# Optimization experiments

Hardware: AMD Instinct MI355X
Metric: run time of the kernel (lower is better)

The kernel has to match this reference:

```python
import jax, jax.numpy as jnp
import numpy as np

B, DIN, H, NACT = 8192, 1025, 1024, 1026
NHEAD = 513  # npatches + STOP
K = 32       # kR = kS


def _make_seq(key, batch, n, k):
    k_idx, k_len = jax.random.split(key)
    # distinct indices per row: top-k of a random permutation
    perm = jnp.argsort(jax.random.uniform(k_idx, (batch, n)), axis=1)[:, :k]
    seq_len = jax.random.randint(k_len, (batch,), 1, k + 1).astype(jnp.int32)
    mask = jnp.arange(k)[None, :] < seq_len[:, None]
    seq_idx = jnp.where(mask, perm, -1).astype(jnp.int32)
    return seq_idx, seq_len


def setup_inputs() -> dict:
    key = jax.random.key(0)
    ks = jax.random.split(key, 8)
    state = jax.random.normal(ks[0], (B, DIN), dtype=jnp.float32)
    W0 = jax.random.normal(ks[1], (DIN, H), dtype=jnp.float32) * (2.0 / DIN) ** 0.5
    b0 = jnp.zeros((H,), jnp.float32)
    W1 = jax.random.normal(ks[2], (H, H), dtype=jnp.float32) * (2.0 / H) ** 0.5
    b1 = jnp.zeros((H,), jnp.float32)
    W2 = jax.random.normal(ks[3], (H, NACT), dtype=jnp.float32) * 0.01
    b2 = jnp.zeros((NACT,), jnp.float32)
    seq_idx_R, seq_len_R = _make_seq(ks[4], B, NHEAD, K)
    seq_idx_S, seq_len_S = _make_seq(ks[5], B, NHEAD, K)
    return {"state": state, "W0": W0, "b0": b0, "W1": W1, "b1": b1,
            "W2": W2, "b2": b2,
            "seq_idx_R": seq_idx_R, "seq_len_R": seq_len_R,
            "seq_idx_S": seq_idx_S, "seq_len_S": seq_len_S}


def _mlp(state, W0, b0, W1, b1, W2, b2):
    h = jax.nn.relu(state @ W0 + b0)
    h = jax.nn.relu(h @ W1 + b1)
    return h @ W2 + b2  # (B, NACT) logits


def _logprob_entropy_wo_replacement(logits, seq_idx, seq_len):
    # Faithful vectorized version of logprob_entropy_wo_replacement_batched.
    bsz, n = logits.shape
    col = jnp.arange(n)[None, :]
    neg_inf = jnp.float32(-jnp.inf)

    def step(carry, xs):
        remaining, logp, ent = carry          # (B,N) bool, (B,), (B,)
        t, idx_t = xs                          # scalar, (B,)
        active = t < seq_len                   # (B,)
        masked_logits = jnp.where(remaining, logits, neg_inf)
        lp = jax.nn.log_softmax(masked_logits, axis=-1)
        p = jnp.exp(lp)
        mp = jnp.where(remaining, p, 0.0)
        mlp_ = jnp.where(remaining, lp, 0.0)
        ent_step = -jnp.sum(mp * mlp_, axis=-1)
        ent = ent + jnp.where(active, ent_step, 0.0)
        valid = active & (idx_t >= 0)
        idx_safe = jnp.where(valid, idx_t, 0)
        g = jnp.take_along_axis(lp, idx_safe[:, None], axis=1)[:, 0]
        logp = logp + jnp.where(valid, g, 0.0)
        hit = (col == idx_safe[:, None]) & valid[:, None]
        remaining = remaining & ~hit
        return (remaining, logp, ent), None

    init = (jnp.ones((bsz, n), bool), jnp.zeros((bsz,), jnp.float32),
            jnp.zeros((bsz,), jnp.float32))
    ts = jnp.arange(seq_idx.shape[1], dtype=jnp.int32)
    (_, logp, ent), _ = jax.lax.scan(step, init, (ts, seq_idx.T))
    return logp, ent


def reference(state, W0, b0, W1, b1, W2, b2,
              seq_idx_R, seq_len_R, seq_idx_S, seq_len_S):
    x = _mlp(state, W0, b0, W1, b1, W2, b2)
    logpR, entR = _logprob_entropy_wo_replacement(x[:, :NHEAD], seq_idx_R, seq_len_R)
    logpS, entS = _logprob_entropy_wo_replacement(x[:, NHEAD:NHEAD + NHEAD], seq_idx_S, seq_len_S)
    # rows: [total logprob, total entropy] as in get_log_prob's (logpR+logpS, entR+entS)
    return jnp.stack([logpR + logpS, entR + entS], axis=0)  # (2, B)
```

## Files before the change

kernel.cpp:

```cpp
#include <hip/hip_runtime.h>
#include <cstdint>
#include <cstddef>

#define BATCH 8192
#define DIN   1025
#define HID   1024
#define NACT  1026
#define NHEAD 513
#define KSEL  32
#define KP0   1088
#define NP2   1152

typedef unsigned short u16;
typedef short bf16x8 __attribute__((ext_vector_type(8)));
typedef float f32x4 __attribute__((ext_vector_type(4)));

__device__ __forceinline__ u16 f2bf(float f) {
  unsigned u = __float_as_uint(f);
  u += 0x7fff + ((u >> 16) & 1);
  return (u16)(u >> 16);
}
__device__ __forceinline__ float bf2f(u16 h) {
  return __uint_as_float((unsigned)h << 16);
}

__device__ __forceinline__ void async_cp16(const u16* g, u16* l) {
  __builtin_amdgcn_global_load_lds((const __attribute__((address_space(1))) void*)g,
                                   (__attribute__((address_space(3))) void*)l,
                                   16, 0, 0);
}


__global__ void cvt_all(const float* __restrict__ state,
                        const float* __restrict__ W0, const float* __restrict__ W1,
                        const float* __restrict__ W2,
                        u16* __restrict__ As, u16* __restrict__ W0t,
                        u16* __restrict__ W1t, u16* __restrict__ W2t) {
  const int b = blockIdx.x;
  const int tid = threadIdx.x;
  if (b < 8704) {
    int idx = b * 256 + tid;
    const int QPR = KP0 / 4;
    int r  = idx / QPR;
    int c4 = (idx - r * QPR) * 4;
    const float* src = state + (size_t)r * DIN + c4;
    ushort4 o;
    if (c4 + 3 < DIN) {
      o.x = f2bf(src[0]); o.y = f2bf(src[1]); o.z = f2bf(src[2]); o.w = f2bf(src[3]);
    } else {
      o.x = (c4 + 0 < DIN) ? f2bf(src[0]) : 0;
      o.y = (c4 + 1 < DIN) ? f2bf(src[1]) : 0;
      o.z = (c4 + 2 < DIN) ? f2bf(src[2]) : 0;
      o.w = (c4 + 3 < DIN) ? f2bf(src[3]) : 0;
    }
    *(ushort4*)(As + (size_t)r * KP0 + c4) = o;
    return;
  }
  int w = b - 8704;
  const float* W; u16* Wt; int K, N, Kp, Np, nx;
  if (w < 1088)      { W = W0; Wt = W0t; K = DIN; N = HID;  Kp = KP0; Np = HID; nx = 32; }
  else if (w < 2112) { w -= 1088; W = W1; Wt = W1t; K = HID; N = HID;  Kp = HID; Np = HID; nx = 32; }
  else               { w -= 2112; W = W2; Wt = W2t; K = HID; N = NACT; Kp = HID; Np = NP2; nx = 36; }
  int n0 = (w % nx) * 32, k0 = (w / nx) * 32;
  __shared__ float tile[32][33];
  int tx = tid & 31, ty = tid >> 5;
#pragma unroll
  for (int i = 0; i < 32; i += 8) {
    int k = k0 + ty + i, n = n0 + tx;
    tile[ty + i][tx] = (k < K && n < N) ? W[(size_t)k * N + n] : 0.f;
  }
  __syncthreads();
#pragma unroll
  for (int i = 0; i < 32; i += 8) {
    int n = n0 + ty + i, k = k0 + tx;
    if (n < Np && k < Kp) Wt[(size_t)n * Kp + k] = f2bf(tile[tx][ty + i]);
  }
}


template<bool RELU, int NT, int K>
__global__ __launch_bounds__(256, 2)
void gemm_bt(const u16* __restrict__ A, const u16* __restrict__ Bt,
             const float* __restrict__ bias, int nbias,
             u16* __restrict__ Cout, int ldc)
{
  __shared__ __align__(16) u16 lds[16384];

  const int d     = blockIdx.x;
  const int group = d / (8 * NT);
  const int rsub  = d - group * (8 * NT);
  const int ntile = rsub >> 3;
  const int mtile = group * 8 + (rsub & 7);

  const int tid  = threadIdx.x;
  const int wave = tid >> 6;
  const int lane = tid & 63;
  const int waveM = wave >> 1, waveN = wave & 1;
  const int lr = lane & 15, lq = lane >> 4;
  const size_t bm = (size_t)mtile * 128;
  const size_t bn = (size_t)ntile * 128;

  const int c0   = wave * 64 + lane;
  const int row0 = c0 >> 2;
  const int g0   = (c0 & 3) ^ ((row0 >> 1) & 3);
  const int c1   = c0 + 256;
  const int row1 = c1 >> 2;
  const int g1   = (c1 & 3) ^ ((row1 >> 1) & 3);
  const u16* gA0 = A  + (bm + row0) * (size_t)K + g0 * 8;
  const u16* gA1 = A  + (bm + row1) * (size_t)K + g1 * 8;
  const u16* gB0 = Bt + (bn + row0) * (size_t)K + g0 * 8;
  const u16* gB1 = Bt + (bn + row1) * (size_t)K + g1 * 8;
  u16* lA = lds + wave * 512;
  u16* lB = lds + 4096 + wave * 512;

  f32x4 acc[4][4] = {};

  const int s = lq ^ ((lr >> 1) & 3);
  const u16* pa = lds + (waveM * 64 + lr) * 32 + s * 8;
  const u16* pb = lds + 4096 + (waveN * 64 + lr) * 32 + s * 8;

  auto issue = [&](int k0, int b) {
    u16* a  = lA + b * 8192;
    u16* bb = lB + b * 8192;
    async_cp16(gA0 + k0, a);
    async_cp16(gA1 + k0, a + 2048);
    async_cp16(gB0 + k0, bb);
    async_cp16(gB1 + k0, bb + 2048);
  };

  const int NIT = K / 32;
  issue(0, 0);
#pragma unroll 2
  for (int it = 0; it < NIT; ++it) {
    const int b = it & 1;
    if (it + 1 < NIT) {
      issue((it + 1) * 32, b ^ 1);
      asm volatile("s_waitcnt vmcnt(4)\n\ts_barrier" ::: "memory");
    } else {
      asm volatile("s_waitcnt vmcnt(0)\n\ts_barrier" ::: "memory");
    }

    bf16x8 af[4], bf[4];
    const u16* qa = pa + b * 8192;
    const u16* qb = pb + b * 8192;
#pragma unroll
    for (int t = 0; t < 4; ++t) {
      af[t] = *(const bf16x8*)(qa + t * 512);
      bf[t] = *(const bf16x8*)(qb + t * 512);
    }
#pragma unroll
    for (int tm = 0; tm < 4; ++tm)
#pragma unroll
      for (int tn = 0; tn < 4; ++tn)
        acc[tm][tn] = __builtin_amdgcn_mfma_f32_16x16x32_bf16(af[tm], bf[tn], acc[tm][tn], 0, 0, 0);

    asm volatile("s_waitcnt lgkmcnt(0)\n\ts_barrier" ::: "memory");
  }

#pragma unroll
  for (int tm = 0; tm < 4; ++tm) {
    size_t rw = bm + waveM * 64 + tm * 16 + lq * 4;
#pragma unroll
    for (int tn = 0; tn < 4; ++tn) {
      int col = (int)bn + waveN * 64 + tn * 16 + lr;
      float bv = (col < nbias) ? bias[col] : 0.f;
#pragma unroll
      for (int r = 0; r < 4; ++r) {
        float v = acc[tm][tn][r] + bv;
        if (RELU) v = fmaxf(v, 0.f);
        Cout[(rw + r) * ldc + col] = f2bf(v);
      }
    }
  }
}


__global__ void sample_k(const u16* __restrict__ logits,
                         const int* __restrict__ idxR, const int* __restrict__ lenR,
                         const int* __restrict__ idxS, const int* __restrict__ lenS,
                         float* __restrict__ out)
{
  const int row  = blockIdx.x;
  const int w    = threadIdx.x >> 6;
  const int lane = threadIdx.x & 63;
  const u16* x = logits + (size_t)row * NP2 + w * NHEAD;
  const int* sidx = (w ? idxS : idxR) + (size_t)row * KSEL;
  const int slen  = (w ? lenS : lenR)[row];

  float m = -3.4e38f;
  for (int i = lane; i < NHEAD; i += 64) m = fmaxf(m, bf2f(x[i]));
#pragma unroll
  for (int d = 32; d; d >>= 1) m = fmaxf(m, __shfl_xor(m, d, 64));

  float S = 0.f, T = 0.f;
  for (int i = lane; i < NHEAD; i += 64) {
    float xi = bf2f(x[i]);
    float e = __expf(xi - m);
    S += e; T += e * xi;
  }
#pragma unroll
  for (int d = 32; d; d >>= 1) { S += __shfl_xor(S, d, 64); T += __shfl_xor(T, d, 64); }

  float e = 0.f, ex = 0.f, xt = 0.f;
  int active = (lane < KSEL) && (lane < slen);
  int valid = 0;
  if (active) {
    int id = sidx[lane];
    if (id >= 0) {
      valid = 1;
      xt = bf2f(x[id]);
      e  = __expf(xt - m);
      ex = e * xt;
    }
  }
  float pe = e, pex = ex;
#pragma unroll
  for (int d = 1; d < 32; d <<= 1) {
    float a = __shfl_up(pe, d, 64);
    float b = __shfl_up(pex, d, 64);
    if (lane >= d) { pe += a; pex += b; }
  }
  float lp = 0.f, en = 0.f;
  if (active) {
    float St = S - (pe - e);
    float Tt = T - (pex - ex);
    float logZ = m + __logf(St);
    en = logZ - Tt / St;
    if (valid) lp = xt - logZ;
  }
#pragma unroll
  for (int d = 32; d; d >>= 1) { lp += __shfl_xor(lp, d, 64); en += __shfl_xor(en, d, 64); }

  __shared__ float sh[4];
  if (lane == 0) { sh[w * 2] = lp; sh[w * 2 + 1] = en; }
  __syncthreads();
  if (threadIdx.x == 0) {
    out[row]         = sh[0] + sh[2];
    out[BATCH + row] = sh[1] + sh[3];
  }
}


extern "C" void kernel_launch(void* const* d_in, const int* in_sizes, int n_in,
                              void* d_out, int out_size, void* d_ws, size_t ws_size,
                              hipStream_t stream) {
  (void)in_sizes; (void)n_in; (void)out_size; (void)ws_size;
  const float* state = (const float*)d_in[0];
  const float* W0 = (const float*)d_in[1];
  const float* b0 = (const float*)d_in[2];
  const float* W1 = (const float*)d_in[3];
  const float* b1 = (const float*)d_in[4];
  const float* W2 = (const float*)d_in[5];
  const float* b2 = (const float*)d_in[6];
  const int* idxR = (const int*)d_in[7];
  const int* lenR = (const int*)d_in[8];
  const int* idxS = (const int*)d_in[9];
  const int* lenS = (const int*)d_in[10];
  float* out = (float*)d_out;

  char* ws = (char*)d_ws;
  size_t off = 0;
  auto alloc = [&](size_t bytes) -> char* {
    char* p = ws + off;
    off = (off + bytes + 255) & ~(size_t)255;
    return p;
  };
  u16* As     = (u16*)alloc((size_t)BATCH * KP0 * 2);
  u16* W0t    = (u16*)alloc((size_t)HID * KP0 * 2);
  u16* W1t    = (u16*)alloc((size_t)HID * HID * 2);
  u16* W2t    = (u16*)alloc((size_t)NP2 * HID * 2);
  u16* h1     = (u16*)alloc((size_t)BATCH * HID * 2);
  u16* lgts   = (u16*)alloc((size_t)BATCH * NP2 * 2);
  u16* h2 = As;

  cvt_all<<<8704 + 3264, 256, 0, stream>>>(state, W0, W1, W2, As, W0t, W1t, W2t);

  gemm_bt<true,  8, KP0><<<(BATCH / 128) * (HID / 128), 256, 0, stream>>>(As, W0t, b0, HID,  h1,   HID);
  gemm_bt<true,  8, HID><<<(BATCH / 128) * (HID / 128), 256, 0, stream>>>(h1, W1t, b1, HID,  h2,   HID);
  gemm_bt<false, 9, HID><<<(BATCH / 128) * (NP2 / 128), 256, 0, stream>>>(h2, W2t, b2, NACT, lgts, NP2);

  sample_k<<<BATCH, 128, 0, stream>>>(lgts, idxR, lenR, idxS, lenS, out);
}
```

Before: 202.3 us.

## Fuse pipeline into persistent cooperative megakernel and compute last two logits in sampler

Replaces the five separate launches (convert, three GEMMs, sampler) with one persistent cooperative kernel of 256 blocks of 512 threads that separates phases with grid syncs. Each block runs two 256-thread GEMM teams on adjacent N tiles. The third GEMM now produces only 1024 logit columns instead of 1152 padded ones, and the two leftover logits are computed as dot products inside the sampling phase. This removes launch gaps and the padded GEMM work. In exchange it relies on cooperative launch (with a multi-kernel fallback), grid-wide barriers, and fixing the GEMM to exactly one tile pair per block.

```diff
diff --git a/kernel.cpp b/kernel.cpp
--- a/kernel.cpp
+++ b/kernel.cpp
@@ -1,6 +1,9 @@
 #include <hip/hip_runtime.h>
+#include <hip/hip_cooperative_groups.h>
 #include <cstdint>
 #include <cstddef>
+
+namespace cg = cooperative_groups;
 
 #define BATCH 8192
 #define DIN   1025
@@ -9,7 +12,8 @@
 #define NHEAD 513
 #define KSEL  32
 #define KP0   1088
-#define NP2   1152
+#define LGN   1024
+#define GRID  256
 
 typedef unsigned short u16;
 typedef short bf16x8 __attribute__((ext_vector_type(8)));
@@ -30,20 +34,19 @@
                                    16, 0, 0);
 }
 
-
-__global__ void cvt_all(const float* __restrict__ state,
-                        const float* __restrict__ W0, const float* __restrict__ W1,
-                        const float* __restrict__ W2,
-                        u16* __restrict__ As, u16* __restrict__ W0t,
-                        u16* __restrict__ W1t, u16* __restrict__ W2t) {
-  const int b = blockIdx.x;
+struct MegaArgs {
+  const float *state, *W0, *b0, *W1, *b1, *W2, *b2;
+  const int *idxR, *lenR, *idxS, *lenS;
+  u16 *As, *W0t, *W1t, *W2t, *W2c, *h1, *h2, *lgts;
+  float *out;
+};
+
+__device__ void cvt_phase(const MegaArgs& a, u16* lds) {
   const int tid = threadIdx.x;
-  if (b < 8704) {
-    int idx = b * 256 + tid;
-    const int QPR = KP0 / 4;
-    int r  = idx / QPR;
-    int c4 = (idx - r * QPR) * 4;
-    const float* src = state + (size_t)r * DIN + c4;
+  const int QPR = KP0 / 4;
+  for (int i = blockIdx.x * 512 + tid; i < BATCH * QPR; i += GRID * 512) {
+    int r = i / QPR, c4 = (i - r * QPR) * 4;
+    const float* src = a.state + (size_t)r * DIN + c4;
     ushort4 o;
     if (c4 + 3 < DIN) {
       o.x = f2bf(src[0]); o.y = f2bf(src[1]); o.z = f2bf(src[2]); o.w = f2bf(src[3]);
@@ -53,52 +56,56 @@
       o.z = (c4 + 2 < DIN) ? f2bf(src[2]) : 0;
       o.w = (c4 + 3 < DIN) ? f2bf(src[3]) : 0;
     }
-    *(ushort4*)(As + (size_t)r * KP0 + c4) = o;
-    return;
-  }
-  int w = b - 8704;
-  const float* W; u16* Wt; int K, N, Kp, Np, nx;
-  if (w < 1088)      { W = W0; Wt = W0t; K = DIN; N = HID;  Kp = KP0; Np = HID; nx = 32; }
-  else if (w < 2112) { w -= 1088; W = W1; Wt = W1t; K = HID; N = HID;  Kp = HID; Np = HID; nx = 32; }
-  else               { w -= 2112; W = W2; Wt = W2t; K = HID; N = NACT; Kp = HID; Np = NP2; nx = 36; }
-  int n0 = (w % nx) * 32, k0 = (w / nx) * 32;
-  __shared__ float tile[32][33];
-  int tx = tid & 31, ty = tid >> 5;
-#pragma unroll
-  for (int i = 0; i < 32; i += 8) {
-    int k = k0 + ty + i, n = n0 + tx;
-    tile[ty + i][tx] = (k < K && n < N) ? W[(size_t)k * N + n] : 0.f;
-  }
-  __syncthreads();
-#pragma unroll
-  for (int i = 0; i < 32; i += 8) {
-    int n = n0 + ty + i, k = k0 + tx;
-    if (n < Np && k < Kp) Wt[(size_t)n * Kp + k] = f2bf(tile[tx][ty + i]);
-  }
-}
-
-
-template<bool RELU, int NT, int K>
-__global__ __launch_bounds__(256, 2)
-void gemm_bt(const u16* __restrict__ A, const u16* __restrict__ Bt,
-             const float* __restrict__ bias, int nbias,
-             u16* __restrict__ Cout, int ldc)
+    *(ushort4*)(a.As + (size_t)r * KP0 + c4) = o;
+  }
+  float (*tile)[33] = (float(*)[33])lds;
+  const int tx = tid & 31, ty = tid >> 5;
+  for (int t = blockIdx.x; t < 3137; t += GRID) {
+    if (t == 3136) {
+      for (int e = tid; e < 2048; e += 512) {
+        int j = e >> 10, k = e & 1023;
+        a.W2c[e] = f2bf(a.W2[(size_t)k * NACT + 1024 + j]);
+      }
+      continue;
+    }
+    const float* W; u16* Wt; int K, ldW, Kp, tt = t;
+    if (tt < 1088)      { W = a.W0; Wt = a.W0t; K = DIN; ldW = HID;  Kp = KP0; }
+    else if (tt < 2112) { tt -= 1088; W = a.W1; Wt = a.W1t; K = HID; ldW = HID;  Kp = HID; }
+    else                { tt -= 2112; W = a.W2; Wt = a.W2t; K = HID; ldW = NACT; Kp = HID; }
+    int n0 = (tt & 31) * 32, k0 = (tt >> 5) * 32;
+#pragma unroll
+    for (int i = 0; i < 32; i += 16) {
+      int k = k0 + ty + i;
+      tile[ty + i][tx] = (k < K) ? W[(size_t)k * ldW + n0 + tx] : 0.f;
+    }
+    __syncthreads();
+#pragma unroll
+    for (int i = 0; i < 32; i += 16)
+      Wt[(size_t)(n0 + ty + i) * Kp + k0 + tx] = f2bf(tile[tx][ty + i]);
+    __syncthreads();
+  }
+}
+
+template<bool RELU, int K>
+__device__ void gemm_phase(const u16* __restrict__ A, const u16* __restrict__ Bt,
+                           const float* __restrict__ bias, u16* __restrict__ Cout,
+                           int ldc, u16* lds0)
 {
-  __shared__ __align__(16) u16 lds[16384];
-
-  const int d     = blockIdx.x;
-  const int group = d / (8 * NT);
-  const int rsub  = d - group * (8 * NT);
-  const int ntile = rsub >> 3;
-  const int mtile = group * 8 + (rsub & 7);
-
   const int tid  = threadIdx.x;
-  const int wave = tid >> 6;
+  const int team = tid >> 8;
+  const int ttid = tid & 255;
+  const int wave = ttid >> 6;
   const int lane = tid & 63;
   const int waveM = wave >> 1, waveN = wave & 1;
   const int lr = lane & 15, lq = lane >> 4;
+
+  const int b = blockIdx.x;
+  const int mtile = ((b >> 5) << 3) | (b & 7);
+  const int ntile = (((b >> 3) & 3) << 1) | team;
   const size_t bm = (size_t)mtile * 128;
   const size_t bn = (size_t)ntile * 128;
+
+  u16* lds = lds0 + team * 16384;
 
   const int c0   = wave * 64 + lane;
   const int row0 = c0 >> 2;
@@ -119,11 +126,11 @@
   const u16* pa = lds + (waveM * 64 + lr) * 32 + s * 8;
   const u16* pb = lds + 4096 + (waveN * 64 + lr) * 32 + s * 8;
 
-  auto issue = [&](int k0, int b) {
-    u16* a  = lA + b * 8192;
-    u16* bb = lB + b * 8192;
-    async_cp16(gA0 + k0, a);
-    async_cp16(gA1 + k0, a + 2048);
+  auto issue = [&](int k0, int buf) {
+    u16* aa = lA + buf * 8192;
+    u16* bb = lB + buf * 8192;
+    async_cp16(gA0 + k0, aa);
+    async_cp16(gA1 + k0, aa + 2048);
     async_cp16(gB0 + k0, bb);
     async_cp16(gB1 + k0, bb + 2048);
   };
@@ -132,17 +139,17 @@
   issue(0, 0);
 #pragma unroll 2
   for (int it = 0; it < NIT; ++it) {
-    const int b = it & 1;
+    const int buf = it & 1;
     if (it + 1 < NIT) {
-      issue((it + 1) * 32, b ^ 1);
+      issue((it + 1) * 32, buf ^ 1);
       asm volatile("s_waitcnt vmcnt(4)\n\ts_barrier" ::: "memory");
     } else {
       asm volatile("s_waitcnt vmcnt(0)\n\ts_barrier" ::: "memory");
     }
 
     bf16x8 af[4], bf[4];
-    const u16* qa = pa + b * 8192;
-    const u16* qb = pb + b * 8192;
+    const u16* qa = pa + buf * 8192;
+    const u16* qb = pb + buf * 8192;
 #pragma unroll
     for (int t = 0; t < 4; ++t) {
       af[t] = *(const bf16x8*)(qa + t * 512);
@@ -163,7 +170,7 @@
 #pragma unroll
     for (int tn = 0; tn < 4; ++tn) {
       int col = (int)bn + waveN * 64 + tn * 16 + lr;
-      float bv = (col < nbias) ? bias[col] : 0.f;
+      float bv = bias[col];
 #pragma unroll
       for (int r = 0; r < 4; ++r) {
         float v = acc[tm][tn][r] + bv;
@@ -174,90 +181,138 @@
   }
 }
 
-
-__global__ void sample_k(const u16* __restrict__ logits,
-                         const int* __restrict__ idxR, const int* __restrict__ lenR,
-                         const int* __restrict__ idxS, const int* __restrict__ lenS,
-                         float* __restrict__ out)
-{
-  const int row  = blockIdx.x;
-  const int w    = threadIdx.x >> 6;
-  const int lane = threadIdx.x & 63;
-  const u16* x = logits + (size_t)row * NP2 + w * NHEAD;
-  const int* sidx = (w ? idxS : idxR) + (size_t)row * KSEL;
-  const int slen  = (w ? lenS : lenR)[row];
-
-  float m = -3.4e38f;
-  for (int i = lane; i < NHEAD; i += 64) m = fmaxf(m, bf2f(x[i]));
-#pragma unroll
-  for (int d = 32; d; d >>= 1) m = fmaxf(m, __shfl_xor(m, d, 64));
-
-  float S = 0.f, T = 0.f;
-  for (int i = lane; i < NHEAD; i += 64) {
-    float xi = bf2f(x[i]);
-    float e = __expf(xi - m);
-    S += e; T += e * xi;
-  }
-#pragma unroll
-  for (int d = 32; d; d >>= 1) { S += __shfl_xor(S, d, 64); T += __shfl_xor(T, d, 64); }
-
-  float e = 0.f, ex = 0.f, xt = 0.f;
-  int active = (lane < KSEL) && (lane < slen);
-  int valid = 0;
-  if (active) {
-    int id = sidx[lane];
-    if (id >= 0) {
-      valid = 1;
-      xt = bf2f(x[id]);
-      e  = __expf(xt - m);
-      ex = e * xt;
-    }
-  }
-  float pe = e, pex = ex;
-#pragma unroll
-  for (int d = 1; d < 32; d <<= 1) {
-    float a = __shfl_up(pe, d, 64);
-    float b = __shfl_up(pex, d, 64);
-    if (lane >= d) { pe += a; pex += b; }
-  }
-  float lp = 0.f, en = 0.f;
-  if (active) {
-    float St = S - (pe - e);
-    float Tt = T - (pex - ex);
-    float logZ = m + __logf(St);
-    en = logZ - Tt / St;
-    if (valid) lp = xt - logZ;
-  }
-#pragma unroll
-  for (int d = 32; d; d >>= 1) { lp += __shfl_xor(lp, d, 64); en += __shfl_xor(en, d, 64); }
-
-  __shared__ float sh[4];
-  if (lane == 0) { sh[w * 2] = lp; sh[w * 2 + 1] = en; }
-  __syncthreads();
-  if (threadIdx.x == 0) {
-    out[row]         = sh[0] + sh[2];
-    out[BATCH + row] = sh[1] + sh[3];
-  }
-}
-
+__device__ void sample_phase(const MegaArgs& a, u16* lds) {
+  float* shf = (float*)lds;
+  const int tid = threadIdx.x;
+  const int w = tid >> 6, lane = tid & 63;
+  const int grp = w & 1, pair = w >> 1;
+  for (int it = 0; it < 8; ++it) {
+    const int row = it * 1024 + blockIdx.x * 4 + pair;
+    const u16* base = a.lgts + (size_t)row * LGN + (grp ? NHEAD : 0);
+    const int* sidx = (grp ? a.idxS : a.idxR) + (size_t)row * KSEL;
+    const int slen  = (grp ? a.lenS : a.lenR)[row];
+
+    float x1024 = 0.f, x1025 = 0.f;
+    if (grp) {
+      float d0 = 0.f, d1 = 0.f;
+      const u16* hr  = a.h2 + (size_t)row * HID + lane * 16;
+      const u16* w0p = a.W2c + lane * 16;
+      const u16* w1p = a.W2c + 1024 + lane * 16;
+#pragma unroll
+      for (int j = 0; j < 16; ++j) {
+        float h = bf2f(hr[j]);
+        d0 += h * bf2f(w0p[j]);
+        d1 += h * bf2f(w1p[j]);
+      }
+#pragma unroll
+      for (int dd = 32; dd; dd >>= 1) { d0 += __shfl_xor(d0, dd, 64); d1 += __shfl_xor(d1, dd, 64); }
+      x1024 = d0 + a.b2[1024];
+      x1025 = d1 + a.b2[1025];
+    }
+    const int NHm = grp ? 511 : 513;
+
+    float m = -3.4e38f;
+    for (int i = lane; i < NHm; i += 64) m = fmaxf(m, bf2f(base[i]));
+    if (grp) {
+      if (lane == 63) m = fmaxf(m, x1024);
+      if (lane == 0)  m = fmaxf(m, x1025);
+    }
+#pragma unroll
+    for (int dd = 32; dd; dd >>= 1) m = fmaxf(m, __shfl_xor(m, dd, 64));
+
+    float S = 0.f, T = 0.f;
+    for (int i = lane; i < NHm; i += 64) {
+      float xi = bf2f(base[i]);
+      float e = __expf(xi - m);
+      S += e; T += e * xi;
+    }
+    if (grp) {
+      if (lane == 63) { float e = __expf(x1024 - m); S += e; T += e * x1024; }
+      if (lane == 0)  { float e = __expf(x1025 - m); S += e; T += e * x1025; }
+    }
+#pragma unroll
+    for (int dd = 32; dd; dd >>= 1) { S += __shfl_xor(S, dd, 64); T += __shfl_xor(T, dd, 64); }
+
+    float e = 0.f, ex = 0.f, xt = 0.f;
+    int active = (lane < KSEL) && (lane < slen);
+    int valid = 0;
+    if (active) {
+      int id = sidx[lane];
+      if (id >= 0) {
+        valid = 1;
+        if (grp && id >= 511) xt = (id == 511) ? x1024 : x1025;
+        else                  xt = bf2f(base[id]);
+        e  = __expf(xt - m);
+        ex = e * xt;
+      }
+    }
+    float pe = e, pex = ex;
+#pragma unroll
+    for (int dd = 1; dd < 32; dd <<= 1) {
+      float qa = __shfl_up(pe, dd, 64);
+      float qb = __shfl_up(pex, dd, 64);
+      if (lane >= dd) { pe += qa; pex += qb; }
+    }
+    float lp = 0.f, en = 0.f;
+    if (active) {
+      float St = S - (pe - e);
+      float Tt = T - (pex - ex);
+      float logZ = m + __logf(St);
+      en = logZ - Tt / St;
+      if (valid) lp = xt - logZ;
+    }
+#pragma unroll
+    for (int dd = 32; dd; dd >>= 1) { lp += __shfl_xor(lp, dd, 64); en += __shfl_xor(en, dd, 64); }
+
+    if (lane == 0) { shf[w * 2] = lp; shf[w * 2 + 1] = en; }
+    __syncthreads();
+    if (lane == 0 && grp == 0) {
+      a.out[row]         = shf[pair * 4] + shf[pair * 4 + 2];
+      a.out[BATCH + row] = shf[pair * 4 + 1] + shf[pair * 4 + 3];
+    }
+    __syncthreads();
+  }
+}
+
+__global__ __launch_bounds__(512, 2) void mega(MegaArgs a) {
+  __shared__ __align__(16) u16 lds[32768];
+  cg::grid_group g = cg::this_grid();
+  cvt_phase(a, lds);
+  __threadfence(); g.sync();
+  gemm_phase<true,  KP0>(a.As, a.W0t, a.b0, a.h1, HID, lds);
+  __threadfence(); g.sync();
+  gemm_phase<true,  HID>(a.h1, a.W1t, a.b1, a.h2, HID, lds);
+  __threadfence(); g.sync();
+  gemm_phase<false, HID>(a.h2, a.W2t, a.b2, a.lgts, LGN, lds);
+  __threadfence(); g.sync();
+  sample_phase(a, lds);
+}
+
+__global__ __launch_bounds__(512, 2) void k_cvt(MegaArgs a) {
+  __shared__ __align__(16) u16 lds[32768];
+  cvt_phase(a, lds);
+}
+__global__ __launch_bounds__(512, 2) void k_gemm1(MegaArgs a) {
+  __shared__ __align__(16) u16 lds[32768];
+  gemm_phase<true, KP0>(a.As, a.W0t, a.b0, a.h1, HID, lds);
+}
+__global__ __launch_bounds__(512, 2) void k_gemm2(MegaArgs a) {
+  __shared__ __align__(16) u16 lds[32768];
+  gemm_phase<true, HID>(a.h1, a.W1t, a.b1, a.h2, HID, lds);
+}
+__global__ __launch_bounds__(512, 2) void k_gemm3(MegaArgs a) {
+  __shared__ __align__(16) u16 lds[32768];
+  gemm_phase<false, HID>(a.h2, a.W2t, a.b2, a.lgts, LGN, lds);
+}
+__global__ __launch_bounds__(512, 2) void k_sample(MegaArgs a) {
+  __shared__ __align__(16) u16 lds[32768];
+  sample_phase(a, lds);
+}
 
 extern "C" void kernel_launch(void* const* d_in, const int* in_sizes, int n_in,
                               void* d_out, int out_size, void* d_ws, size_t ws_size,
                               hipStream_t stream) {
   (void)in_sizes; (void)n_in; (void)out_size; (void)ws_size;
-  const float* state = (const float*)d_in[0];
-  const float* W0 = (const float*)d_in[1];
-  const float* b0 = (const float*)d_in[2];
-  const float* W1 = (const float*)d_in[3];
-  const float* b1 = (const float*)d_in[4];
-  const float* W2 = (const float*)d_in[5];
-  const float* b2 = (const float*)d_in[6];
-  const int* idxR = (const int*)d_in[7];
-  const int* lenR = (const int*)d_in[8];
-  const int* idxS = (const int*)d_in[9];
-  const int* lenS = (const int*)d_in[10];
-  float* out = (float*)d_out;
-
   char* ws = (char*)d_ws;
   size_t off = 0;
   auto alloc = [&](size_t bytes) -> char* {
@@ -265,19 +320,34 @@
     off = (off + bytes + 255) & ~(size_t)255;
     return p;
   };
-  u16* As     = (u16*)alloc((size_t)BATCH * KP0 * 2);
-  u16* W0t    = (u16*)alloc((size_t)HID * KP0 * 2);
-  u16* W1t    = (u16*)alloc((size_t)HID * HID * 2);
-  u16* W2t    = (u16*)alloc((size_t)NP2 * HID * 2);
-  u16* h1     = (u16*)alloc((size_t)BATCH * HID * 2);
-  u16* lgts   = (u16*)alloc((size_t)BATCH * NP2 * 2);
-  u16* h2 = As;
-
-  cvt_all<<<8704 + 3264, 256, 0, stream>>>(state, W0, W1, W2, As, W0t, W1t, W2t);
-
-  gemm_bt<true,  8, KP0><<<(BATCH / 128) * (HID / 128), 256, 0, stream>>>(As, W0t, b0, HID,  h1,   HID);
-  gemm_bt<true,  8, HID><<<(BATCH / 128) * (HID / 128), 256, 0, stream>>>(h1, W1t, b1, HID,  h2,   HID);
-  gemm_bt<false, 9, HID><<<(BATCH / 128) * (NP2 / 128), 256, 0, stream>>>(h2, W2t, b2, NACT, lgts, NP2);
-
-  sample_k<<<BATCH, 128, 0, stream>>>(lgts, idxR, lenR, idxS, lenS, out);
-}
+
+  MegaArgs a;
+  a.state = (const float*)d_in[0];
+  a.W0 = (const float*)d_in[1];  a.b0 = (const float*)d_in[2];
+  a.W1 = (const float*)d_in[3];  a.b1 = (const float*)d_in[4];
+  a.W2 = (const float*)d_in[5];  a.b2 = (const float*)d_in[6];
+  a.idxR = (const int*)d_in[7];  a.lenR = (const int*)d_in[8];
+  a.idxS = (const int*)d_in[9];  a.lenS = (const int*)d_in[10];
+  a.out = (float*)d_out;
+
+  a.As   = (u16*)alloc((size_t)BATCH * KP0 * 2);
+  a.W0t  = (u16*)alloc((size_t)HID * KP0 * 2);
+  a.W1t  = (u16*)alloc((size_t)HID * HID * 2);
+  a.W2t  = (u16*)alloc((size_t)HID * LGN * 2);
+  a.W2c  = (u16*)alloc((size_t)2 * 1024 * 2);
+  a.h1   = (u16*)alloc((size_t)BATCH * HID * 2);
+  a.h2   = (u16*)alloc((size_t)BATCH * HID * 2);
+  a.lgts = (u16*)alloc((size_t)BATCH * LGN * 2);
+
+  void* params[] = { &a };
+  hipError_t err = hipLaunchCooperativeKernel((const void*)mega, dim3(GRID), dim3(512),
+                                              params, 0, stream);
+  if (err != hipSuccess) {
+    (void)hipGetLastError();
+    k_cvt   <<<GRID, 512, 0, stream>>>(a);
+    k_gemm1 <<<GRID, 512, 0, stream>>>(a);
+    k_gemm2 <<<GRID, 512, 0, stream>>>(a);
+    k_gemm3 <<<GRID, 512, 0, stream>>>(a);
+    k_sample<<<GRID, 512, 0, stream>>>(a);
+  }
+}
```

Result: slower. 596.8 us (+194.9%).

## Use 128x256 GEMM tiles and compute the last two logits in the sampling kernel

Applied to the files above, without the earlier changes.

The GEMM moves to 512-thread blocks that each compute a 128x256 output tile with a larger double-buffered LDS, so the launch is 256 blocks instead of 512. The final GEMM's N dimension shrinks from a padded 1152 to 1024. The two leftover logit columns (1024 and 1025) are computed as small dot products inside the sampling kernel, which now handles four rows per block. The aim is to cut padded GEMM work and raise operand reuse per tile. The cost is a single wave of large blocks on the GPU, which may leave compute units idle or unbalanced, plus extra per-row dot-product work in the sampler.

```diff
diff --git a/kernel.cpp b/kernel.cpp
--- a/kernel.cpp
+++ b/kernel.cpp
@@ -9,7 +9,7 @@
 #define NHEAD 513
 #define KSEL  32
 #define KP0   1088
-#define NP2   1152
+#define LGN   1024
 
 typedef unsigned short u16;
 typedef short bf16x8 __attribute__((ext_vector_type(8)));
@@ -30,19 +30,17 @@
                                    16, 0, 0);
 }
 
-
-__global__ void cvt_all(const float* __restrict__ state,
-                        const float* __restrict__ W0, const float* __restrict__ W1,
-                        const float* __restrict__ W2,
-                        u16* __restrict__ As, u16* __restrict__ W0t,
-                        u16* __restrict__ W1t, u16* __restrict__ W2t) {
+__global__ __launch_bounds__(512) void k_cvt(const float* __restrict__ state,
+    const float* __restrict__ W0, const float* __restrict__ W1,
+    const float* __restrict__ W2,
+    u16* __restrict__ As, u16* __restrict__ W0t, u16* __restrict__ W1t,
+    u16* __restrict__ W2t, u16* __restrict__ W2c) {
+  const int tid = threadIdx.x;
   const int b = blockIdx.x;
-  const int tid = threadIdx.x;
-  if (b < 8704) {
-    int idx = b * 256 + tid;
+  {
+    int i = b * 512 + tid;
     const int QPR = KP0 / 4;
-    int r  = idx / QPR;
-    int c4 = (idx - r * QPR) * 4;
+    int r = i / QPR, c4 = (i - r * QPR) * 4;
     const float* src = state + (size_t)r * DIN + c4;
     ushort4 o;
     if (c4 + 3 < DIN) {
@@ -54,64 +52,65 @@
       o.w = (c4 + 3 < DIN) ? f2bf(src[3]) : 0;
     }
     *(ushort4*)(As + (size_t)r * KP0 + c4) = o;
+  }
+  if (b >= 3137) return;
+  if (b == 3136) {
+    for (int e = tid; e < 2048; e += 512) {
+      int j = e >> 10, k = e & 1023;
+      W2c[e] = f2bf(W2[(size_t)k * NACT + 1024 + j]);
+    }
     return;
   }
-  int w = b - 8704;
-  const float* W; u16* Wt; int K, N, Kp, Np, nx;
-  if (w < 1088)      { W = W0; Wt = W0t; K = DIN; N = HID;  Kp = KP0; Np = HID; nx = 32; }
-  else if (w < 2112) { w -= 1088; W = W1; Wt = W1t; K = HID; N = HID;  Kp = HID; Np = HID; nx = 32; }
-  else               { w -= 2112; W = W2; Wt = W2t; K = HID; N = NACT; Kp = HID; Np = NP2; nx = 36; }
-  int n0 = (w % nx) * 32, k0 = (w / nx) * 32;
+  const float* W; u16* Wt; int K, ldW, Kp, tt = b;
+  if (tt < 1088)      { W = W0; Wt = W0t; K = DIN; ldW = HID;  Kp = KP0; }
+  else if (tt < 2112) { tt -= 1088; W = W1; Wt = W1t; K = HID; ldW = HID;  Kp = HID; }
+  else                { tt -= 2112; W = W2; Wt = W2t; K = HID; ldW = NACT; Kp = HID; }
+  int n0 = (tt & 31) * 32, k0 = (tt >> 5) * 32;
   __shared__ float tile[32][33];
-  int tx = tid & 31, ty = tid >> 5;
-#pragma unroll
-  for (int i = 0; i < 32; i += 8) {
-    int k = k0 + ty + i, n = n0 + tx;
-    tile[ty + i][tx] = (k < K && n < N) ? W[(size_t)k * N + n] : 0.f;
+  const int tx = tid & 31, ty = tid >> 5;
+#pragma unroll
+  for (int i = 0; i < 32; i += 16) {
+    int k = k0 + ty + i;
+    tile[ty + i][tx] = (k < K) ? W[(size_t)k * ldW + n0 + tx] : 0.f;
   }
   __syncthreads();
 #pragma unroll
-  for (int i = 0; i < 32; i += 8) {
-    int n = n0 + ty + i, k = k0 + tx;
-    if (n < Np && k < Kp) Wt[(size_t)n * Kp + k] = f2bf(tile[tx][ty + i]);
-  }
-}
-
-
-template<bool RELU, int NT, int K>
-__global__ __launch_bounds__(256, 2)
+  for (int i = 0; i < 32; i += 16)
+    Wt[(size_t)(n0 + ty + i) * Kp + k0 + tx] = f2bf(tile[tx][ty + i]);
+}
+
+template<bool RELU, int K>
+__global__ __launch_bounds__(512, 2)
 void gemm_bt(const u16* __restrict__ A, const u16* __restrict__ Bt,
-             const float* __restrict__ bias, int nbias,
-             u16* __restrict__ Cout, int ldc)
+             const float* __restrict__ bias, u16* __restrict__ Cout, int ldc)
 {
-  __shared__ __align__(16) u16 lds[16384];
+  __shared__ __align__(16) u16 lds[24576];
 
   const int d     = blockIdx.x;
-  const int group = d / (8 * NT);
-  const int rsub  = d - group * (8 * NT);
-  const int ntile = rsub >> 3;
-  const int mtile = group * 8 + (rsub & 7);
+  const int m8    = d & 7;
+  const int ntile = (d >> 3) & 3;
+  const int mtile = ((d >> 5) << 3) | m8;
+  const size_t bm = (size_t)mtile * 128;
+  const size_t bn = (size_t)ntile * 256;
 
   const int tid  = threadIdx.x;
   const int wave = tid >> 6;
   const int lane = tid & 63;
-  const int waveM = wave >> 1, waveN = wave & 1;
+  const int waveM = wave >> 2, waveN = wave & 3;
   const int lr = lane & 15, lq = lane >> 4;
-  const size_t bm = (size_t)mtile * 128;
-  const size_t bn = (size_t)ntile * 128;
-
-  const int c0   = wave * 64 + lane;
-  const int row0 = c0 >> 2;
-  const int g0   = (c0 & 3) ^ ((row0 >> 1) & 3);
-  const int c1   = c0 + 256;
-  const int row1 = c1 >> 2;
-  const int g1   = (c1 & 3) ^ ((row1 >> 1) & 3);
-  const u16* gA0 = A  + (bm + row0) * (size_t)K + g0 * 8;
-  const u16* gA1 = A  + (bm + row1) * (size_t)K + g1 * 8;
-  const u16* gB0 = Bt + (bn + row0) * (size_t)K + g0 * 8;
-  const u16* gB1 = Bt + (bn + row1) * (size_t)K + g1 * 8;
-  u16* lA = lds + wave * 512;
-  u16* lB = lds + 4096 + wave * 512;
+
+  const int rowA  = tid >> 2;
+  const int gA_   = (tid & 3) ^ ((rowA >> 1) & 3);
+  const int rowB0 = tid >> 2;
+  const int gB0_  = (tid & 3) ^ ((rowB0 >> 1) & 3);
+  const int rowB1 = rowB0 + 128;
+  const int gB1_  = (tid & 3) ^ ((rowB1 >> 1) & 3);
+  const u16* gA  = A  + (bm + rowA)  * (size_t)K + gA_  * 8;
+  const u16* gB0 = Bt + (bn + rowB0) * (size_t)K + gB0_ * 8;
+  const u16* gB1 = Bt + (bn + rowB1) * (size_t)K + gB1_ * 8;
+  u16* lA  = lds + wave * 512;
+  u16* lB0 = lds + 4096 + wave * 512;
+  u16* lB1 = lB0 + 4096;
 
   f32x4 acc[4][4] = {};
 
@@ -119,30 +118,28 @@
   const u16* pa = lds + (waveM * 64 + lr) * 32 + s * 8;
   const u16* pb = lds + 4096 + (waveN * 64 + lr) * 32 + s * 8;
 
-  auto issue = [&](int k0, int b) {
-    u16* a  = lA + b * 8192;
-    u16* bb = lB + b * 8192;
-    async_cp16(gA0 + k0, a);
-    async_cp16(gA1 + k0, a + 2048);
-    async_cp16(gB0 + k0, bb);
-    async_cp16(gB1 + k0, bb + 2048);
+  auto issue = [&](int k0, int buf) {
+    const int o = buf * 12288;
+    async_cp16(gA  + k0, lA  + o);
+    async_cp16(gB0 + k0, lB0 + o);
+    async_cp16(gB1 + k0, lB1 + o);
   };
 
   const int NIT = K / 32;
   issue(0, 0);
 #pragma unroll 2
   for (int it = 0; it < NIT; ++it) {
-    const int b = it & 1;
+    const int buf = it & 1;
     if (it + 1 < NIT) {
-      issue((it + 1) * 32, b ^ 1);
-      asm volatile("s_waitcnt vmcnt(4)\n\ts_barrier" ::: "memory");
+      issue((it + 1) * 32, buf ^ 1);
+      asm volatile("s_waitcnt vmcnt(3)\n\ts_barrier" ::: "memory");
     } else {
       asm volatile("s_waitcnt vmcnt(0)\n\ts_barrier" ::: "memory");
     }
 
     bf16x8 af[4], bf[4];
-    const u16* qa = pa + b * 8192;
-    const u16* qb = pb + b * 8192;
+    const u16* qa = pa + buf * 12288;
+    const u16* qb = pb + buf * 12288;
 #pragma unroll
     for (int t = 0; t < 4; ++t) {
       af[t] = *(const bf16x8*)(qa + t * 512);
@@ -163,7 +160,7 @@
 #pragma unroll
     for (int tn = 0; tn < 4; ++tn) {
       int col = (int)bn + waveN * 64 + tn * 16 + lr;
-      float bv = (col < nbias) ? bias[col] : 0.f;
+      float bv = bias[col];
 #pragma unroll
       for (int r = 0; r < 4; ++r) {
         float v = acc[tm][tn][r] + bv;
@@ -174,32 +171,61 @@
   }
 }
 
-
-__global__ void sample_k(const u16* __restrict__ logits,
-                         const int* __restrict__ idxR, const int* __restrict__ lenR,
-                         const int* __restrict__ idxS, const int* __restrict__ lenS,
-                         float* __restrict__ out)
-{
-  const int row  = blockIdx.x;
-  const int w    = threadIdx.x >> 6;
-  const int lane = threadIdx.x & 63;
-  const u16* x = logits + (size_t)row * NP2 + w * NHEAD;
-  const int* sidx = (w ? idxS : idxR) + (size_t)row * KSEL;
-  const int slen  = (w ? lenS : lenR)[row];
+__global__ __launch_bounds__(512) void k_sample(const u16* __restrict__ lgts,
+    const u16* __restrict__ h2, const u16* __restrict__ W2c,
+    const float* __restrict__ b2,
+    const int* __restrict__ idxR, const int* __restrict__ lenR,
+    const int* __restrict__ idxS, const int* __restrict__ lenS,
+    float* __restrict__ out) {
+  __shared__ float shf[16];
+  const int tid = threadIdx.x;
+  const int w = tid >> 6, lane = tid & 63;
+  const int grp = w & 1, pair = w >> 1;
+  const int row = blockIdx.x * 4 + pair;
+  const u16* base = lgts + (size_t)row * LGN + (grp ? NHEAD : 0);
+  const int* sidx = (grp ? idxS : idxR) + (size_t)row * KSEL;
+  const int slen  = (grp ? lenS : lenR)[row];
+
+  float x1024 = 0.f, x1025 = 0.f;
+  if (grp) {
+    float d0 = 0.f, d1 = 0.f;
+    const u16* hr  = h2 + (size_t)row * HID + lane * 16;
+    const u16* w0p = W2c + lane * 16;
+    const u16* w1p = W2c + 1024 + lane * 16;
+#pragma unroll
+    for (int j = 0; j < 16; ++j) {
+      float h = bf2f(hr[j]);
+      d0 += h * bf2f(w0p[j]);
+      d1 += h * bf2f(w1p[j]);
+    }
+#pragma unroll
+    for (int dd = 32; dd; dd >>= 1) { d0 += __shfl_xor(d0, dd, 64); d1 += __shfl_xor(d1, dd, 64); }
+    x1024 = d0 + b2[1024];
+    x1025 = d1 + b2[1025];
+  }
+  const int NHm = grp ? 511 : 513;
 
   float m = -3.4e38f;
-  for (int i = lane; i < NHEAD; i += 64) m = fmaxf(m, bf2f(x[i]));
-#pragma unroll
-  for (int d = 32; d; d >>= 1) m = fmaxf(m, __shfl_xor(m, d, 64));
+  for (int i = lane; i < NHm; i += 64) m = fmaxf(m, bf2f(base[i]));
+  if (grp) {
+    if (lane == 63) m = fmaxf(m, x1024);
+    if (lane == 0)  m = fmaxf(m, x1025);
+  }
+#pragma unroll
+  for (int dd = 32; dd; dd >>= 1) m = fmaxf(m, __shfl_xor(m, dd, 64));
 
   float S = 0.f, T = 0.f;
-  for (int i = lane; i < NHEAD; i += 64) {
-    float xi = bf2f(x[i]);
+  for (int i = lane; i < NHm; i += 64) {
+    float xi = bf2f(base[i]);
     float e = __expf(xi - m);
     S += e; T += e * xi;
   }
-#pragma unroll
-  for (int d = 32; d; d >>= 1) { S += __shfl_xor(S, d, 64); T += __shfl_xor(T, d, 64); }
+  if (grp) {
+    if (lane == 63) { float e = __expf(x1024 - m); S += e; T += e * x1024; }
+    if (lane == 0)  { float e = __expf(x1025 - m); S += e; T += e * x1025; }
+  }
+#pragma unroll
+  for (int dd = 32; dd; dd >>= 1) { S += __shfl_xor(S, dd, 64); T += __shfl_xor(T, dd, 64); }
 
   float e = 0.f, ex = 0.f, xt = 0.f;
   int active = (lane < KSEL) && (lane < slen);
@@ -208,17 +234,18 @@
     int id = sidx[lane];
     if (id >= 0) {
       valid = 1;
-      xt = bf2f(x[id]);
+      if (grp && id >= 511) xt = (id == 511) ? x1024 : x1025;
+      else                  xt = bf2f(base[id]);
       e  = __expf(xt - m);
       ex = e * xt;
     }
   }
   float pe = e, pex = ex;
 #pragma unroll
-  for (int d = 1; d < 32; d <<= 1) {
-    float a = __shfl_up(pe, d, 64);
-    float b = __shfl_up(pex, d, 64);
-    if (lane >= d) { pe += a; pex += b; }
+  for (int dd = 1; dd < 32; dd <<= 1) {
+    float qa = __shfl_up(pe, dd, 64);
+    float qb = __shfl_up(pex, dd, 64);
+    if (lane >= dd) { pe += qa; pex += qb; }
   }
   float lp = 0.f, en = 0.f;
   if (active) {
@@ -229,17 +256,15 @@
     if (valid) lp = xt - logZ;
   }
 #pragma unroll
-  for (int d = 32; d; d >>= 1) { lp += __shfl_xor(lp, d, 64); en += __shfl_xor(en, d, 64); }
-
-  __shared__ float sh[4];
-  if (lane == 0) { sh[w * 2] = lp; sh[w * 2 + 1] = en; }
+  for (int dd = 32; dd; dd >>= 1) { lp += __shfl_xor(lp, dd, 64); en += __shfl_xor(en, dd, 64); }
+
+  if (lane == 0) { shf[w * 2] = lp; shf[w * 2 + 1] = en; }
   __syncthreads();
-  if (threadIdx.x == 0) {
-    out[row]         = sh[0] + sh[2];
-    out[BATCH + row] = sh[1] + sh[3];
-  }
-}
-
+  if (lane == 0 && grp == 0) {
+    out[row]         = shf[pair * 4] + shf[pair * 4 + 2];
+    out[BATCH + row] = shf[pair * 4 + 1] + shf[pair * 4 + 3];
+  }
+}
 
 extern "C" void kernel_launch(void* const* d_in, const int* in_sizes, int n_in,
                               void* d_out, int out_size, void* d_ws, size_t ws_size,
@@ -265,19 +290,20 @@
     off = (off + bytes + 255) & ~(size_t)255;
     return p;
   };
-  u16* As     = (u16*)alloc((size_t)BATCH * KP0 * 2);
-  u16* W0t    = (u16*)alloc((size_t)HID * KP0 * 2);
-  u16* W1t    = (u16*)alloc((size_t)HID * HID * 2);
-  u16* W2t    = (u16*)alloc((size_t)NP2 * HID * 2);
-  u16* h1     = (u16*)alloc((size_t)BATCH * HID * 2);
-  u16* lgts   = (u16*)alloc((size_t)BATCH * NP2 * 2);
-  u16* h2 = As;
-
-  cvt_all<<<8704 + 3264, 256, 0, stream>>>(state, W0, W1, W2, As, W0t, W1t, W2t);
-
-  gemm_bt<true,  8, KP0><<<(BATCH / 128) * (HID / 128), 256, 0, stream>>>(As, W0t, b0, HID,  h1,   HID);
-  gemm_bt<true,  8, HID><<<(BATCH / 128) * (HID / 128), 256, 0, stream>>>(h1, W1t, b1, HID,  h2,   HID);
-  gemm_bt<false, 9, HID><<<(BATCH / 128) * (NP2 / 128), 256, 0, stream>>>(h2, W2t, b2, NACT, lgts, NP2);
-
-  sample_k<<<BATCH, 128, 0, stream>>>(lgts, idxR, lenR, idxS, lenS, out);
-}
+  u16* As   = (u16*)alloc((size_t)BATCH * KP0 * 2);
+  u16* W0t  = (u16*)alloc((size_t)HID * KP0 * 2);
+  u16* W1t  = (u16*)alloc((size_t)HID * HID * 2);
+  u16* W2t  = (u16*)alloc((size_t)HID * LGN * 2);
+  u16* W2c  = (u16*)alloc((size_t)2 * 1024 * 2);
+  u16* h1   = (u16*)alloc((size_t)BATCH * HID * 2);
+  u16* h2   = (u16*)alloc((size_t)BATCH * HID * 2);
+  u16* lgts = (u16*)alloc((size_t)BATCH * LGN * 2);
+
+  k_cvt<<<4352, 512, 0, stream>>>(state, W0, W1, W2, As, W0t, W1t, W2t, W2c);
+
+  gemm_bt<true,  KP0><<<256, 512, 0, stream>>>(As, W0t, b0, h1,   HID);
+  gemm_bt<true,  HID><<<256, 512, 0, stream>>>(h1, W1t, b1, h2,   HID);
+  gemm_bt<false, HID><<<256, 512, 0, stream>>>(h2, W2t, b2, lgts, LGN);
+
+  k_sample<<<2048, 512, 0, stream>>>(lgts, h2, W2c, b2, idxR, lenR, idxS, lenS, out);
+}
```

Measured after the change: 194.4 us. 1.04x faster.
